# Kernel tuning notes

Hardware: AMD Instinct MI355X
Metric: run time of the kernel (lower is better)

Reference implementation:

```python
import jax, jax.numpy as jnp
import numpy as np
from jax import lax
from jax.scipy.special import logsumexp

TEMP_MIN, TEMP_MAX = 0.1, 1.0
B, I, J, C = 2, 128, 512, 256


def setup_inputs() -> dict:
    key = jax.random.key(0)
    k1, k2, k3 = jax.random.split(key, 3)
    return {
        "text_embeddings": jax.random.normal(k1, (B, I, C), dtype=jnp.float32),
        "mel_embeddings": jax.random.normal(k2, (B, J, C), dtype=jnp.float32),
        "text_mask": jnp.ones((B, I), dtype=jnp.float32),
        "mel_mask": jnp.ones((B, J), dtype=jnp.float32),
        "noise": jax.random.gumbel(k3, (B, I, J), dtype=jnp.float32),  # -log(-log(U))
        "temperature_ratio": jnp.float32(0.5),
    }


def _cond_prob(energy, text_mask, mel_mask, direction):
    # energy: [B, I, J]; returns [B, I, J, K] log conditional probs (normalized over axis 2)
    b, i, j = energy.shape
    if direction == "alpha":
        k = j
        tri = jnp.arange(j)[:, None] >= jnp.arange(k)[None, :]  # triu(ones(J,J)).T layout -> j >= k
        mel_k = mel_mask
    else:  # beta
        k = j - 1
        tri = jnp.arange(j)[:, None] <= jnp.arange(k)[None, :]  # tril(ones(J-1,J)).T layout -> j <= k
        mel_k = mel_mask[:, :k]
    valid = (
        (text_mask[:, :, None, None] * mel_mask[:, None, :, None] * mel_k[:, None, None, :]) > 0
    ) & tri[None, None]
    e4 = jnp.where(valid, energy[..., None], -jnp.inf)  # [B,I,J,K]
    e4 = e4 - logsumexp(e4, axis=2, keepdims=True)
    return jnp.where(valid, e4, jnp.asarray(-10.0, energy.dtype))


def reference(text_embeddings, mel_embeddings, text_mask, mel_mask, noise, temperature_ratio):
    b, i_len, ct = text_embeddings.shape
    j_len, cm = mel_embeddings.shape[1], mel_embeddings.shape[2]
    ninf = jnp.asarray(-jnp.inf, text_embeddings.dtype)

    energy = jnp.einsum("bic,bjc->bij", text_embeddings, mel_embeddings) / np.sqrt(ct * cm)
    temperature = TEMP_MIN + (TEMP_MAX - TEMP_MIN) * temperature_ratio
    energy = (energy + noise) / temperature

    cpa = _cond_prob(energy, text_mask, mel_mask, "alpha")  # [B,I,J,J]
    cpb = _cond_prob(energy, text_mask, mel_mask, "beta")   # [B,I,J,J-1]

    # forward (alpha) recursion over text dim: alpha[:, i, j+1] = LSE_k(alpha[:, i-1, k] + cpa[:, i-1, j, k])
    init_a = jnp.full((b, j_len + 1), -jnp.inf, energy.dtype).at[:, 0].set(0.0)

    def astep(carry, cpa_i):  # carry [B, J+1], cpa_i [B, J, J]
        row = logsumexp(carry[:, None, :-1] + cpa_i, axis=2)  # [B, J]
        new = jnp.concatenate([jnp.full((b, 1), -jnp.inf, energy.dtype), row], axis=1)
        return new, row

    _, arows = lax.scan(astep, init_a, jnp.swapaxes(cpa, 0, 1))
    alpha = jnp.swapaxes(arows, 0, 1)  # [B, I, J] == alpha[:, 1:, 1:]

    # backward (beta) recursion: beta[:, i, j] = LSE_k(beta[:, i+1, k+1] + cpb[:, i, j, k])
    init_b = jnp.full((b, j_len), -jnp.inf, energy.dtype).at[:, -1].set(0.0)

    def bstep(carry, cpb_i):  # carry [B, J], cpb_i [B, J, J-1]
        row = logsumexp(carry[:, None, 1:] + cpb_i, axis=2)
        return row, row

    _, brows = lax.scan(bstep, init_b, jnp.flip(jnp.swapaxes(cpb[:, : i_len - 1], 0, 1), axis=0))
    beta = jnp.concatenate([jnp.flip(brows, axis=0), init_b[None]], axis=0)
    beta = jnp.swapaxes(beta, 0, 1)  # [B, I, J]

    gamma = alpha + beta
    gmask = (text_mask[:, :, None] * mel_mask[:, None, :]) > 0
    gamma = jnp.where(gmask, gamma, ninf)
    gamma = jnp.where(gmask, gamma - logsumexp(gamma, axis=1, keepdims=True), ninf)

    expanded = jnp.einsum("bij,bic->bjc", jnp.exp(gamma), text_embeddings)
    expanded = expanded * mel_mask[:, :, None]
    return gamma, expanded
```

## Files before the change

### kernel.cpp

```cpp
#include <hip/hip_runtime.h>
#include <math.h>

#define BB 2
#define II 128
#define JJ 512
#define CC 256
#define NEL (BB*II*JJ)
#define NINF (-INFINITY)
#define K10 4.5399929762484854e-5f

typedef float f32x4 __attribute__((ext_vector_type(4)));

template<int CTRL, int RM = 0xf, int BM = 0xf, bool BC = true>
__device__ __forceinline__ float dppf(float x) {
    return __int_as_float(__builtin_amdgcn_update_dpp(
        0, __float_as_int(x), CTRL, RM, BM, BC));
}
template<int CTRL, int RM = 0xf, int BM = 0xf>
__device__ __forceinline__ float dppself(float x) {
    return __int_as_float(__builtin_amdgcn_update_dpp(
        __float_as_int(x), __float_as_int(x), CTRL, RM, BM, false));
}
__device__ __forceinline__ float wscan_incl(float x) {
    x += dppf<0x111>(x);
    x += dppf<0x112>(x);
    x += dppf<0x114>(x);
    x += dppf<0x118>(x);
    x += dppf<0x142, 0xa>(x);
    x += dppf<0x143, 0xc>(x);
    return x;
}
__device__ __forceinline__ float wscan_maxf(float x) {
    x = fmaxf(x, dppself<0x111>(x));
    x = fmaxf(x, dppself<0x112>(x));
    x = fmaxf(x, dppself<0x114>(x));
    x = fmaxf(x, dppself<0x118>(x));
    x = fmaxf(x, dppself<0x142, 0xa>(x));
    x = fmaxf(x, dppself<0x143, 0xc>(x));
    return x;
}
__device__ __forceinline__ float lane_shr1(float x) { return dppf<0x138>(x); }
__device__ __forceinline__ float bcast63(float x) {
    return __int_as_float(__builtin_amdgcn_readlane(__float_as_int(x), 63));
}

__device__ __forceinline__ void tree_prefix8(const float x[8], float P[8]) {
    float t[8];
    t[0] = x[0];
    #pragma unroll
    for (int q = 1; q < 8; ++q) t[q] = x[q] + x[q-1];
    float u[8];
    u[0] = t[0]; u[1] = t[1];
    #pragma unroll
    for (int q = 2; q < 8; ++q) u[q] = t[q] + t[q-2];
    P[0] = u[0]; P[1] = u[1]; P[2] = u[2]; P[3] = u[3];
    #pragma unroll
    for (int q = 4; q < 8; ++q) P[q] = u[q] + u[q-4];
}

__device__ __forceinline__ void loadrow8(const float* p, float v[8]) {
    float4 a = *reinterpret_cast<const float4*>(p);
    float4 b = *reinterpret_cast<const float4*>(p + 4);
    v[0]=a.x; v[1]=a.y; v[2]=a.z; v[3]=a.w;
    v[4]=b.x; v[5]=b.y; v[6]=b.z; v[7]=b.w;
}
__device__ __forceinline__ void storerow8(float* __restrict__ p, const float v[8]) {
    *reinterpret_cast<float4*>(p)     = make_float4(v[0],v[1],v[2],v[3]);
    *reinterpret_cast<float4*>(p + 4) = make_float4(v[4],v[5],v[6],v[7]);
}

__device__ __forceinline__ void aload2(f32x4 &d0, f32x4 &d1, const float* p) {
    asm volatile("global_load_dwordx4 %0, %2, off\n\t"
                 "global_load_dwordx4 %1, %2, off offset:16"
                 : "=&v"(d0), "=&v"(d1) : "v"(p) : "memory");
}
__device__ __forceinline__ void astore2(f32x4 d0, f32x4 d1, float* p) {
    asm volatile("global_store_dwordx4 %2, %0, off\n\t"
                 "global_store_dwordx4 %2, %1, off offset:16"
                 :: "v"(d0), "v"(d1), "v"(p) : "memory");
}
template<int N> __device__ __forceinline__ void waitcnt_vm() {
    asm volatile("s_waitcnt vmcnt(%0)" :: "i"(N) : "memory");
}

struct Buf { f32x4 e0, e1; };

__device__ __forceinline__ void preproc(const float ev[8], float CE[8], float CW[8]) {
    float m8 = fmaxf(fmaxf(fmaxf(ev[0],ev[1]), fmaxf(ev[2],ev[3])),
                     fmaxf(fmaxf(ev[4],ev[5]), fmaxf(ev[6],ev[7])));
    float m = bcast63(wscan_maxf(m8));
    float x[8];
    #pragma unroll
    for (int q = 0; q < 8; ++q) x[q] = __expf(ev[q] - m);
    float P[8];
    tree_prefix8(x, P);
    float sc = wscan_incl(P[7]);
    float cp = lane_shr1(sc);
    float T  = bcast63(sc);
    #pragma unroll
    for (int q = 0; q < 8; ++q) {
        CE[q] = x[q];
        CW[q] = __builtin_amdgcn_rcpf(T - (cp + P[q]) + x[q]);
    }
}

__global__ __launch_bounds__(256) void energy_kernel(
        const float* __restrict__ text, const float* __restrict__ mel,
        const float* __restrict__ noise, const float* __restrict__ ratio,
        float* __restrict__ e) {
    __shared__ float melS[64][65];
    __shared__ float texS[8][65];
    int b  = blockIdx.x;
    int i0 = blockIdx.y * 8;
    int j0 = blockIdx.z * 64;
    int t = threadIdx.x;
    int jj = t & 63, ig = t >> 6;
    float acc0 = 0.f, acc1 = 0.f;
    for (int cc = 0; cc < CC; cc += 64) {
        #pragma unroll
        for (int k = 0; k < 4; ++k) {
            int idx = t + k * 256;
            int row = idx >> 4, seg = idx & 15;
            float4 v = *reinterpret_cast<const float4*>(
                mel + (size_t)(b * JJ + j0 + row) * CC + cc + seg * 4);
            melS[row][seg*4+0] = v.x; melS[row][seg*4+1] = v.y;
            melS[row][seg*4+2] = v.z; melS[row][seg*4+3] = v.w;
        }
        if (t < 128) {
            int row = t >> 4, seg = t & 15;
            float4 v = *reinterpret_cast<const float4*>(
                text + (size_t)(b * II + i0 + row) * CC + cc + seg * 4);
            texS[row][seg*4+0] = v.x; texS[row][seg*4+1] = v.y;
            texS[row][seg*4+2] = v.z; texS[row][seg*4+3] = v.w;
        }
        __syncthreads();
        #pragma unroll 8
        for (int c = 0; c < 64; ++c) {
            float m = melS[jj][c];
            acc0 = fmaf(m, texS[ig*2+0][c], acc0);
            acc1 = fmaf(m, texS[ig*2+1][c], acc1);
        }
        __syncthreads();
    }
    float temp = 0.1f + 0.9f * ratio[0];
    float rtmp = 1.0f / temp;
    int r0 = (b * II + i0 + ig*2 + 0) * JJ + j0 + jj;
    int r1 = (b * II + i0 + ig*2 + 1) * JJ + j0 + jj;
    e[r0] = (acc0 * (1.0f/256.0f) + noise[r0]) * rtmp;
    e[r1] = (acc1 * (1.0f/256.0f) + noise[r1]) * rtmp;
}


template<bool NORM, int VM, bool PF>
__device__ __forceinline__ void astep(
    int i, int lane, int off,
    const float (&pin)[8], float (&pout)[8], float& c,
    Buf& B,
    const float* __restrict__ eB,
    float* __restrict__ paB, float* ldsC)
{
    {
        f32x4 s0 = {pin[0], pin[1], pin[2], pin[3]};
        f32x4 s1 = {pin[4], pin[5], pin[6], pin[7]};
        astore2(s0, s1, paB + (size_t)(i - 1) * JJ + off);
    }
    if (lane == 0) ldsC[i - 1] = c;
    waitcnt_vm<VM>();
    __builtin_amdgcn_sched_barrier(0);
    float ev[8] = {B.e0[0],B.e0[1],B.e0[2],B.e0[3],B.e1[0],B.e1[1],B.e1[2],B.e1[3]};
    if (PF) aload2(B.e0, B.e1, eB + (size_t)(i + 5) * JJ + off);
    float CE[8], CW[8];
    preproc(ev, CE, CW);

    float pup = lane_shr1(pin[7]);
    float y[8];
    y[0] = pup * CW[0];
    #pragma unroll
    for (int q = 1; q < 8; ++q) y[q] = pin[q-1] * CW[q];
    float zz[8];
    #pragma unroll
    for (int q = 0; q < 7; ++q) zz[q] = pin[q];
    zz[7] = (lane == 63) ? 0.0f : pin[7];
    float Y[8], Z[8];
    tree_prefix8(y, Y);
    tree_prefix8(zz, Z);
    float sy = wscan_incl(Y[7]);
    float sz = wscan_incl(Z[7]);
    float oy = lane_shr1(sy);
    float oz = lane_shr1(sz);
    float T  = bcast63(sz);
    #pragma unroll
    for (int q = 0; q < 8; ++q) {
        float S1 = oy + Y[q];
        float S2 = fmaxf(T - (oz + Z[q]) + zz[q], 0.0f);
        pout[q] = fmaf(CE[q], S1, K10 * S2);
    }
    if (NORM) {
        float Tc = fmaxf(T, 1e-30f);
        float rT = __builtin_amdgcn_rcpf(Tc);
        c += __logf(Tc);
        #pragma unroll
        for (int q = 0; q < 8; ++q) pout[q] *= rT;
    }
}

template<bool NORM, int VM, bool PF>
__device__ __forceinline__ void bstep(
    int i, int lane, int off,
    const float (&pin)[8], float (&pout)[8], float& c,
    Buf& B,
    const float* __restrict__ eB,
    float* __restrict__ pbB, float* ldsC)
{
    {
        f32x4 s0 = {pin[0], pin[1], pin[2], pin[3]};
        f32x4 s1 = {pin[4], pin[5], pin[6], pin[7]};
        astore2(s0, s1, pbB + (size_t)(i + 1) * JJ + off);
    }
    if (lane == 0) ldsC[i + 1] = c;
    waitcnt_vm<VM>();
    __builtin_amdgcn_sched_barrier(0);
    float ev[8] = {B.e1[3],B.e1[2],B.e1[1],B.e1[0],B.e0[3],B.e0[2],B.e0[1],B.e0[0]};
    if (PF) aload2(B.e0, B.e1, eB + (size_t)(i - 5) * JJ + 504 - 8 * lane);
    float CE[8], CW[8];
    preproc(ev, CE, CW);

    float pup = lane_shr1(pin[7]);
    float pn[8];
    pn[0] = pup;
    #pragma unroll
    for (int q = 1; q < 8; ++q) pn[q] = pin[q-1];
    float w[8];
    #pragma unroll
    for (int q = 0; q < 8; ++q) w[q] = pn[q] * CW[q];
    float W[8], N[8];
    tree_prefix8(w, W);
    tree_prefix8(pn, N);
    float sw = wscan_incl(W[7]);
    float sn = wscan_incl(N[7]);
    float ow = lane_shr1(sw);
    float on = lane_shr1(sn);
    float T  = bcast63(sn);
    #pragma unroll
    for (int q = 0; q < 8; ++q) {
        float QA = ow + W[q];
        float QB = fmaxf(T - (on + N[q]), 0.0f);
        pout[q] = fmaf(CE[q], QA, K10 * QB);
    }
    if (NORM) {
        float Tc = fmaxf(T, 1e-30f);
        float rT = __builtin_amdgcn_rcpf(Tc);
        c += __logf(Tc);
        #pragma unroll
        for (int q = 0; q < 8; ++q) pout[q] *= rT;
    }
}

__global__ __launch_bounds__(64, 1) void scan_ab_kernel(
        const float* __restrict__ e,
        float* __restrict__ pa, float* __restrict__ pb,
        float* __restrict__ ca, float* __restrict__ cb) {
    __shared__ float ldsC[II];
    int b = blockIdx.x >> 1, dir = blockIdx.x & 1;
    int lane = threadIdx.x, off = lane * 8;
    size_t base = (size_t)b * II * JJ;
    float PS0[8],PS1[8],PS2[8],PS3[8],PS4[8],PS5[8],PS6[8],PS7[8],PS8[8],PS9[8];
    Buf B0,B1,B2,B3,B4;
    float c = 0.0f;

    if (dir == 0) {
        const float* eB = e + base;
        float* paB = pa + base; float* caB = ca + b * II;
        float e0r[8];
        loadrow8(eB + off, e0r);
        {
            float m8 = fmaxf(fmaxf(fmaxf(e0r[0],e0r[1]), fmaxf(e0r[2],e0r[3])),
                             fmaxf(fmaxf(e0r[4],e0r[5]), fmaxf(e0r[6],e0r[7])));
            float m = bcast63(wscan_maxf(m8));
            float x0[8];
            #pragma unroll
            for (int q = 0; q < 8; ++q) x0[q] = __expf(e0r[q] - m);
            float P[8];
            tree_prefix8(x0, P);
            float T = bcast63(wscan_incl(P[7]));
            float rT = __builtin_amdgcn_rcpf(T);
            #pragma unroll
            for (int q = 0; q < 8; ++q) PS0[q] = x0[q] * rT;
        }
        __builtin_amdgcn_sched_barrier(0);
        aload2(B1.e0, B1.e1, eB + (size_t)1*JJ + off);
        aload2(B2.e0, B2.e1, eB + (size_t)2*JJ + off);
        aload2(B3.e0, B3.e1, eB + (size_t)3*JJ + off);
        aload2(B4.e0, B4.e1, eB + (size_t)4*JJ + off);
        aload2(B0.e0, B0.e1, eB + (size_t)5*JJ + off);
        astep<true ,10,true>(1, lane, off, PS0, PS1, c, B1, eB, paB, ldsC);
        astep<false,12,true>(2, lane, off, PS1, PS2, c, B2, eB, paB, ldsC);
        astep<false,14,true>(3, lane, off, PS2, PS3, c, B3, eB, paB, ldsC);
        astep<false,16,true>(4, lane, off, PS3, PS4, c, B4, eB, paB, ldsC);
        astep<false,18,true>(5, lane, off, PS4, PS5, c, B0, eB, paB, ldsC);
        #pragma unroll 1
        for (int d = 0; d < 11; ++d) {
            int i = 6 + 10 * d;
            astep<true ,18,true>(i+0, lane, off, PS5, PS6, c, B1, eB, paB, ldsC);
            astep<false,18,true>(i+1, lane, off, PS6, PS7, c, B2, eB, paB, ldsC);
            astep<false,18,true>(i+2, lane, off, PS7, PS8, c, B3, eB, paB, ldsC);
            astep<false,18,true>(i+3, lane, off, PS8, PS9, c, B4, eB, paB, ldsC);
            astep<false,18,true>(i+4, lane, off, PS9, PS0, c, B0, eB, paB, ldsC);
            astep<true ,18,true>(i+5, lane, off, PS0, PS1, c, B1, eB, paB, ldsC);
            astep<false,18,true>(i+6, lane, off, PS1, PS2, c, B2, eB, paB, ldsC);
            astep<false,18,true>(i+7, lane, off, PS2, PS3, c, B3, eB, paB, ldsC);
            astep<false,18,true>(i+8, lane, off, PS3, PS4, c, B4, eB, paB, ldsC);
            astep<false,18,true>(i+9, lane, off, PS4, PS5, c, B0, eB, paB, ldsC);
        }
        astep<true ,18,true>(116, lane, off, PS5, PS6, c, B1, eB, paB, ldsC);
        astep<false,18,true>(117, lane, off, PS6, PS7, c, B2, eB, paB, ldsC);
        astep<false,18,true>(118, lane, off, PS7, PS8, c, B3, eB, paB, ldsC);
        astep<false,18,true>(119, lane, off, PS8, PS9, c, B4, eB, paB, ldsC);
        astep<false,18,true>(120, lane, off, PS9, PS0, c, B0, eB, paB, ldsC);
        astep<true ,18,true>(121, lane, off, PS0, PS1, c, B1, eB, paB, ldsC);
        astep<false,18,true>(122, lane, off, PS1, PS2, c, B2, eB, paB, ldsC);
        astep<false,18,false>(123, lane, off, PS2, PS3, c, B3, eB, paB, ldsC);
        astep<false,16,false>(124, lane, off, PS3, PS4, c, B4, eB, paB, ldsC);
        astep<false,14,false>(125, lane, off, PS4, PS5, c, B0, eB, paB, ldsC);
        astep<true ,12,false>(126, lane, off, PS5, PS6, c, B1, eB, paB, ldsC);
        astep<false,10,false>(127, lane, off, PS6, PS7, c, B2, eB, paB, ldsC);
        storerow8(paB + (size_t)127 * JJ + off, PS7);
        if (lane == 0) ldsC[127] = c;
        waitcnt_vm<0>();
        caB[lane]      = ldsC[lane];
        caB[lane + 64] = ldsC[lane + 64];
    } else {
        const float* eB = e + base;
        float* pbB = pb + base; float* cbB = cb + b * II;
        #pragma unroll
        for (int q = 0; q < 8; ++q) PS7[q] = 0.0f;
        PS7[0] = (lane == 0) ? 1.0f : 0.0f;
        aload2(B1.e0, B1.e1, eB + (size_t)126*JJ + 504 - 8*lane);
        aload2(B0.e0, B0.e1, eB + (size_t)125*JJ + 504 - 8*lane);
        aload2(B4.e0, B4.e1, eB + (size_t)124*JJ + 504 - 8*lane);
        aload2(B3.e0, B3.e1, eB + (size_t)123*JJ + 504 - 8*lane);
        aload2(B2.e0, B2.e1, eB + (size_t)122*JJ + 504 - 8*lane);
        bstep<true ,10,true>(126, lane, off, PS7, PS6, c, B1, eB, pbB, ldsC);
        bstep<false,12,true>(125, lane, off, PS6, PS5, c, B0, eB, pbB, ldsC);
        bstep<false,14,true>(124, lane, off, PS5, PS4, c, B4, eB, pbB, ldsC);
        bstep<false,16,true>(123, lane, off, PS4, PS3, c, B3, eB, pbB, ldsC);
        bstep<false,18,true>(122, lane, off, PS3, PS2, c, B2, eB, pbB, ldsC);
        #pragma unroll 1
        for (int d = 0; d < 11; ++d) {
            int i = 121 - 10 * d;
            bstep<true ,18,true>(i-0, lane, off, PS2, PS1, c, B1, eB, pbB, ldsC);
            bstep<false,18,true>(i-1, lane, off, PS1, PS0, c, B0, eB, pbB, ldsC);
            bstep<false,18,true>(i-2, lane, off, PS0, PS9, c, B4, eB, pbB, ldsC);
            bstep<false,18,true>(i-3, lane, off, PS9, PS8, c, B3, eB, pbB, ldsC);
            bstep<false,18,true>(i-4, lane, off, PS8, PS7, c, B2, eB, pbB, ldsC);
            bstep<true ,18,true>(i-5, lane, off, PS7, PS6, c, B1, eB, pbB, ldsC);
            bstep<false,18,true>(i-6, lane, off, PS6, PS5, c, B0, eB, pbB, ldsC);
            bstep<false,18,true>(i-7, lane, off, PS5, PS4, c, B4, eB, pbB, ldsC);
            bstep<false,18,true>(i-8, lane, off, PS4, PS3, c, B3, eB, pbB, ldsC);
            bstep<false,18,true>(i-9, lane, off, PS3, PS2, c, B2, eB, pbB, ldsC);
        }
        bstep<true ,18,true>(11, lane, off, PS2, PS1, c, B1, eB, pbB, ldsC);
        bstep<false,18,true>(10, lane, off, PS1, PS0, c, B0, eB, pbB, ldsC);
        bstep<false,18,true>( 9, lane, off, PS0, PS9, c, B4, eB, pbB, ldsC);
        bstep<false,18,true>( 8, lane, off, PS9, PS8, c, B3, eB, pbB, ldsC);
        bstep<false,18,true>( 7, lane, off, PS8, PS7, c, B2, eB, pbB, ldsC);
        bstep<true ,18,true>( 6, lane, off, PS7, PS6, c, B1, eB, pbB, ldsC);
        bstep<false,18,true>( 5, lane, off, PS6, PS5, c, B0, eB, pbB, ldsC);
        bstep<false,18,false>(4, lane, off, PS5, PS4, c, B4, eB, pbB, ldsC);
        bstep<false,16,false>(3, lane, off, PS4, PS3, c, B3, eB, pbB, ldsC);
        bstep<false,14,false>(2, lane, off, PS3, PS2, c, B2, eB, pbB, ldsC);
        bstep<true ,12,false>(1, lane, off, PS2, PS1, c, B1, eB, pbB, ldsC);
        bstep<false,10,false>(0, lane, off, PS1, PS0, c, B0, eB, pbB, ldsC);
        storerow8(pbB + off, PS0);
        if (lane == 0) ldsC[0] = c;
        waitcnt_vm<0>();
        cbB[lane]      = ldsC[lane];
        cbB[lane + 64] = ldsC[lane + 64];
    }
}

__global__ __launch_bounds__(256) void gamma_expand_kernel(
        const float* __restrict__ pa, const float* __restrict__ pb,
        const float* __restrict__ ca, const float* __restrict__ cb,
        const float* __restrict__ text, const float* __restrict__ mmask,
        float* __restrict__ gamma_out, float* __restrict__ expanded) {
    __shared__ float wt[II][9];
    __shared__ float Ei[II];
    __shared__ float red[8][33];
    int b   = blockIdx.x >> 6;
    int jj0 = (blockIdx.x & 63) * 8;
    int t = threadIdx.x;
    int q = t & 7, ic = t >> 3;

    if (t < II) Ei[t] = ca[b*II + t] + cb[b*II + t];
    __syncthreads();
    float maxc = Ei[0];
    #pragma unroll 16
    for (int i = 1; i < II; ++i) maxc = fmaxf(maxc, Ei[i]);
    __syncthreads();
    if (t < II) Ei[t] = __expf(Ei[t] - maxc);
    __syncthreads();

    size_t idx0  = (size_t)b * II * JJ + jj0 + q;
    size_t idx0r = (size_t)b * II * JJ + (JJ - 1 - jj0 - q);
    float d = 0.f;
    #pragma unroll
    for (int k = 0; k < 4; ++k) {
        int i = ic * 4 + k;
        float P = pa[idx0 + (size_t)i * JJ] * pb[idx0r + (size_t)i * JJ] * Ei[i];
        wt[i][q] = P;
        d += P;
    }
    red[q][ic] = d;
    __syncthreads();
    if (t < 8) {
        float s = 0.f;
        #pragma unroll
        for (int k = 0; k < 32; ++k) s += red[t][k];
        red[t][32] = 1.0f / fmaxf(s, 1e-37f);
    }
    __syncthreads();
    float rD = red[q][32];
    #pragma unroll
    for (int k = 0; k < 4; ++k) {
        int i = ic * 4 + k;
        float P = wt[i][q] * rD;
        wt[i][q] = P;
        gamma_out[idx0 + (size_t)i * JJ] = fmaxf(__logf(P), -1e30f);
    }
    __syncthreads();

    float acc[8] = {0,0,0,0,0,0,0,0};
    const float* txb = text + (size_t)b * II * CC + t;
    #pragma unroll 4
    for (int i = 0; i < II; ++i) {
        float tv = txb[(size_t)i * CC];
        #pragma unroll
        for (int qq = 0; qq < 8; ++qq) acc[qq] = fmaf(wt[i][qq], tv, acc[qq]);
    }
    #pragma unroll
    for (int qq = 0; qq < 8; ++qq) {
        expanded[(size_t)(b * JJ + jj0 + qq) * CC + t] =
            acc[qq] * mmask[b * JJ + jj0 + qq];
    }
}

extern "C" void kernel_launch(void* const* d_in, const int* in_sizes, int n_in,
                              void* d_out, int out_size, void* d_ws, size_t ws_size,
                              hipStream_t stream) {
    const float* text  = (const float*)d_in[0];
    const float* mel   = (const float*)d_in[1];
    const float* mmask = (const float*)d_in[3];
    const float* noise = (const float*)d_in[4];
    const float* ratio = (const float*)d_in[5];
    float* gamma_out = (float*)d_out;
    float* expanded  = (float*)d_out + NEL;

    float* ws = (float*)d_ws;
    float* e  = ws;
    float* pa = ws +   NEL;
    float* pb = ws + 2*NEL;
    float* ca = ws + 3*NEL;
    float* cb = ws + 3*NEL + BB*II;

    hipLaunchKernelGGL(energy_kernel, dim3(BB, II/8, JJ/64), dim3(256), 0, stream,
                       text, mel, noise, ratio, e);
    hipLaunchKernelGGL(scan_ab_kernel, dim3(BB*2), dim3(64), 0, stream,
                       e, pa, pb, ca, cb);
    hipLaunchKernelGGL(gamma_expand_kernel, dim3(BB*64), dim3(256), 0, stream,
                       pa, pb, ca, cb, text, mmask, gamma_out, expanded);
}
```

Measured before the change: 156.5 us.

## Software-pipeline energy preprocessing one step ahead and deepen row prefetch to seven

The alpha and beta scan steps now compute the exp-based CE/CW coefficients for the next row while the current row's prefix scan runs, using double-buffered coefficient registers. The prefetch ring grows from five to seven row buffers and the unroll period from ten to fourteen steps, so loads are issued eight rows ahead. This takes the exp preprocessing and load latency off the serial dependency chain at the cost of more live VGPRs, which could cause spills in a one-wave-per-block kernel.

After: 156.6 us. Within noise of the previous version (+0.1%).

```diff
diff --git a/kernel.cpp b/kernel.cpp
--- a/kernel.cpp
+++ b/kernel.cpp
@@ -151,11 +151,13 @@
 }
 
 
-template<bool NORM, int VM, bool PF>
+template<bool NORM, int VM, bool PF, bool PP>
 __device__ __forceinline__ void astep(
     int i, int lane, int off,
     const float (&pin)[8], float (&pout)[8], float& c,
     Buf& B,
+    const float (&CEc)[8], const float (&CWc)[8],
+    float (&CEn)[8], float (&CWn)[8],
     const float* __restrict__ eB,
     float* __restrict__ paB, float* ldsC)
 {
@@ -165,18 +167,23 @@
         astore2(s0, s1, paB + (size_t)(i - 1) * JJ + off);
     }
     if (lane == 0) ldsC[i - 1] = c;
-    waitcnt_vm<VM>();
-    __builtin_amdgcn_sched_barrier(0);
-    float ev[8] = {B.e0[0],B.e0[1],B.e0[2],B.e0[3],B.e1[0],B.e1[1],B.e1[2],B.e1[3]};
-    if (PF) aload2(B.e0, B.e1, eB + (size_t)(i + 5) * JJ + off);
-    float CE[8], CW[8];
-    preproc(ev, CE, CW);
+    if constexpr (VM >= 0) {
+        waitcnt_vm<VM>();
+        __builtin_amdgcn_sched_barrier(0);
+    }
+    float ev[8];
+    if (PP) {
+        ev[0]=B.e0[0]; ev[1]=B.e0[1]; ev[2]=B.e0[2]; ev[3]=B.e0[3];
+        ev[4]=B.e1[0]; ev[5]=B.e1[1]; ev[6]=B.e1[2]; ev[7]=B.e1[3];
+    }
+    if (PF) aload2(B.e0, B.e1, eB + (size_t)(i + 8) * JJ + off);
+    if (PP) preproc(ev, CEn, CWn);
 
     float pup = lane_shr1(pin[7]);
     float y[8];
-    y[0] = pup * CW[0];
-    #pragma unroll
-    for (int q = 1; q < 8; ++q) y[q] = pin[q-1] * CW[q];
+    y[0] = pup * CWc[0];
+    #pragma unroll
+    for (int q = 1; q < 8; ++q) y[q] = pin[q-1] * CWc[q];
     float zz[8];
     #pragma unroll
     for (int q = 0; q < 7; ++q) zz[q] = pin[q];
@@ -193,7 +200,7 @@
     for (int q = 0; q < 8; ++q) {
         float S1 = oy + Y[q];
         float S2 = fmaxf(T - (oz + Z[q]) + zz[q], 0.0f);
-        pout[q] = fmaf(CE[q], S1, K10 * S2);
+        pout[q] = fmaf(CEc[q], S1, K10 * S2);
     }
     if (NORM) {
         float Tc = fmaxf(T, 1e-30f);
@@ -204,11 +211,13 @@
     }
 }
 
-template<bool NORM, int VM, bool PF>
+template<bool NORM, int VM, bool PF, bool PP>
 __device__ __forceinline__ void bstep(
     int i, int lane, int off,
     const float (&pin)[8], float (&pout)[8], float& c,
     Buf& B,
+    const float (&CEc)[8], const float (&CWc)[8],
+    float (&CEn)[8], float (&CWn)[8],
     const float* __restrict__ eB,
     float* __restrict__ pbB, float* ldsC)
 {
@@ -218,12 +227,17 @@
         astore2(s0, s1, pbB + (size_t)(i + 1) * JJ + off);
     }
     if (lane == 0) ldsC[i + 1] = c;
-    waitcnt_vm<VM>();
-    __builtin_amdgcn_sched_barrier(0);
-    float ev[8] = {B.e1[3],B.e1[2],B.e1[1],B.e1[0],B.e0[3],B.e0[2],B.e0[1],B.e0[0]};
-    if (PF) aload2(B.e0, B.e1, eB + (size_t)(i - 5) * JJ + 504 - 8 * lane);
-    float CE[8], CW[8];
-    preproc(ev, CE, CW);
+    if constexpr (VM >= 0) {
+        waitcnt_vm<VM>();
+        __builtin_amdgcn_sched_barrier(0);
+    }
+    float ev[8];
+    if (PP) {
+        ev[0]=B.e1[3]; ev[1]=B.e1[2]; ev[2]=B.e1[1]; ev[3]=B.e1[0];
+        ev[4]=B.e0[3]; ev[5]=B.e0[2]; ev[6]=B.e0[1]; ev[7]=B.e0[0];
+    }
+    if (PF) aload2(B.e0, B.e1, eB + (size_t)(i - 8) * JJ + 504 - 8 * lane);
+    if (PP) preproc(ev, CEn, CWn);
 
     float pup = lane_shr1(pin[7]);
     float pn[8];
@@ -232,7 +246,7 @@
     for (int q = 1; q < 8; ++q) pn[q] = pin[q-1];
     float w[8];
     #pragma unroll
-    for (int q = 0; q < 8; ++q) w[q] = pn[q] * CW[q];
+    for (int q = 0; q < 8; ++q) w[q] = pn[q] * CWc[q];
     float W[8], N[8];
     tree_prefix8(w, W);
     tree_prefix8(pn, N);
@@ -245,7 +259,7 @@
     for (int q = 0; q < 8; ++q) {
         float QA = ow + W[q];
         float QB = fmaxf(T - (on + N[q]), 0.0f);
-        pout[q] = fmaf(CE[q], QA, K10 * QB);
+        pout[q] = fmaf(CEc[q], QA, K10 * QB);
     }
     if (NORM) {
         float Tc = fmaxf(T, 1e-30f);
@@ -264,8 +278,10 @@
     int b = blockIdx.x >> 1, dir = blockIdx.x & 1;
     int lane = threadIdx.x, off = lane * 8;
     size_t base = (size_t)b * II * JJ;
-    float PS0[8],PS1[8],PS2[8],PS3[8],PS4[8],PS5[8],PS6[8],PS7[8],PS8[8],PS9[8];
-    Buf B0,B1,B2,B3,B4;
+    float PS0[8],PS1[8],PS2[8],PS3[8],PS4[8],PS5[8],PS6[8],PS7[8],
+          PS8[8],PS9[8],PS10[8],PS11[8],PS12[8],PS13[8];
+    Buf B0,B1,B2,B3,B4,B5,B6;
+    float CEa[8], CWa[8], CEb[8], CWb[8];
     float c = 0.0f;
 
     if (dir == 0) {
@@ -292,39 +308,50 @@
         aload2(B2.e0, B2.e1, eB + (size_t)2*JJ + off);
         aload2(B3.e0, B3.e1, eB + (size_t)3*JJ + off);
         aload2(B4.e0, B4.e1, eB + (size_t)4*JJ + off);
-        aload2(B0.e0, B0.e1, eB + (size_t)5*JJ + off);
-        astep<true ,10,true>(1, lane, off, PS0, PS1, c, B1, eB, paB, ldsC);
-        astep<false,12,true>(2, lane, off, PS1, PS2, c, B2, eB, paB, ldsC);
-        astep<false,14,true>(3, lane, off, PS2, PS3, c, B3, eB, paB, ldsC);
-        astep<false,16,true>(4, lane, off, PS3, PS4, c, B4, eB, paB, ldsC);
-        astep<false,18,true>(5, lane, off, PS4, PS5, c, B0, eB, paB, ldsC);
+        aload2(B5.e0, B5.e1, eB + (size_t)5*JJ + off);
+        aload2(B6.e0, B6.e1, eB + (size_t)6*JJ + off);
+        aload2(B0.e0, B0.e1, eB + (size_t)7*JJ + off);
+        waitcnt_vm<0>();
+        __builtin_amdgcn_sched_barrier(0);
+        {
+            float ev[8] = {B1.e0[0],B1.e0[1],B1.e0[2],B1.e0[3],B1.e1[0],B1.e1[1],B1.e1[2],B1.e1[3]};
+            aload2(B1.e0, B1.e1, eB + (size_t)8*JJ + off);
+            preproc(ev, CEb, CWb);
+        }
+        astep<true , 4,true,true>(1, lane, off, PS0, PS1, c, B2, CEb,CWb, CEa,CWa, eB, paB, ldsC);
+        astep<false, 8,true,true>(2, lane, off, PS1, PS2, c, B3, CEa,CWa, CEb,CWb, eB, paB, ldsC);
+        astep<false,12,true,true>(3, lane, off, PS2, PS3, c, B4, CEb,CWb, CEa,CWa, eB, paB, ldsC);
+        astep<false,16,true,true>(4, lane, off, PS3, PS4, c, B5, CEa,CWa, CEb,CWb, eB, paB, ldsC);
+        astep<false,20,true,true>(5, lane, off, PS4, PS5, c, B6, CEb,CWb, CEa,CWa, eB, paB, ldsC);
+        astep<false,24,true,true>(6, lane, off, PS5, PS6, c, B0, CEa,CWa, CEb,CWb, eB, paB, ldsC);
+        astep<false,26,true,true>(7, lane, off, PS6, PS7, c, B1, CEb,CWb, CEa,CWa, eB, paB, ldsC);
         #pragma unroll 1
-        for (int d = 0; d < 11; ++d) {
-            int i = 6 + 10 * d;
-            astep<true ,18,true>(i+0, lane, off, PS5, PS6, c, B1, eB, paB, ldsC);
-            astep<false,18,true>(i+1, lane, off, PS6, PS7, c, B2, eB, paB, ldsC);
-            astep<false,18,true>(i+2, lane, off, PS7, PS8, c, B3, eB, paB, ldsC);
-            astep<false,18,true>(i+3, lane, off, PS8, PS9, c, B4, eB, paB, ldsC);
-            astep<false,18,true>(i+4, lane, off, PS9, PS0, c, B0, eB, paB, ldsC);
-            astep<true ,18,true>(i+5, lane, off, PS0, PS1, c, B1, eB, paB, ldsC);
-            astep<false,18,true>(i+6, lane, off, PS1, PS2, c, B2, eB, paB, ldsC);
-            astep<false,18,true>(i+7, lane, off, PS2, PS3, c, B3, eB, paB, ldsC);
-            astep<false,18,true>(i+8, lane, off, PS3, PS4, c, B4, eB, paB, ldsC);
-            astep<false,18,true>(i+9, lane, off, PS4, PS5, c, B0, eB, paB, ldsC);
-        }
-        astep<true ,18,true>(116, lane, off, PS5, PS6, c, B1, eB, paB, ldsC);
-        astep<false,18,true>(117, lane, off, PS6, PS7, c, B2, eB, paB, ldsC);
-        astep<false,18,true>(118, lane, off, PS7, PS8, c, B3, eB, paB, ldsC);
-        astep<false,18,true>(119, lane, off, PS8, PS9, c, B4, eB, paB, ldsC);
-        astep<false,18,true>(120, lane, off, PS9, PS0, c, B0, eB, paB, ldsC);
-        astep<true ,18,true>(121, lane, off, PS0, PS1, c, B1, eB, paB, ldsC);
-        astep<false,18,true>(122, lane, off, PS1, PS2, c, B2, eB, paB, ldsC);
-        astep<false,18,false>(123, lane, off, PS2, PS3, c, B3, eB, paB, ldsC);
-        astep<false,16,false>(124, lane, off, PS3, PS4, c, B4, eB, paB, ldsC);
-        astep<false,14,false>(125, lane, off, PS4, PS5, c, B0, eB, paB, ldsC);
-        astep<true ,12,false>(126, lane, off, PS5, PS6, c, B1, eB, paB, ldsC);
-        astep<false,10,false>(127, lane, off, PS6, PS7, c, B2, eB, paB, ldsC);
-        storerow8(paB + (size_t)127 * JJ + off, PS7);
+        for (int d = 0; d < 8; ++d) {
+            int i = 8 + 14 * d;
+            astep<true ,26,true,true>(i+ 0, lane, off, PS7 , PS8 , c, B2, CEa,CWa, CEb,CWb, eB, paB, ldsC);
+            astep<false,26,true,true>(i+ 1, lane, off, PS8 , PS9 , c, B3, CEb,CWb, CEa,CWa, eB, paB, ldsC);
+            astep<false,26,true,true>(i+ 2, lane, off, PS9 , PS10, c, B4, CEa,CWa, CEb,CWb, eB, paB, ldsC);
+            astep<false,26,true,true>(i+ 3, lane, off, PS10, PS11, c, B5, CEb,CWb, CEa,CWa, eB, paB, ldsC);
+            astep<false,26,true,true>(i+ 4, lane, off, PS11, PS12, c, B6, CEa,CWa, CEb,CWb, eB, paB, ldsC);
+            astep<false,26,true,true>(i+ 5, lane, off, PS12, PS13, c, B0, CEb,CWb, CEa,CWa, eB, paB, ldsC);
+            astep<false,26,true,true>(i+ 6, lane, off, PS13, PS0 , c, B1, CEa,CWa, CEb,CWb, eB, paB, ldsC);
+            astep<true ,26,true,true>(i+ 7, lane, off, PS0 , PS1 , c, B2, CEb,CWb, CEa,CWa, eB, paB, ldsC);
+            astep<false,26,true,true>(i+ 8, lane, off, PS1 , PS2 , c, B3, CEa,CWa, CEb,CWb, eB, paB, ldsC);
+            astep<false,26,true,true>(i+ 9, lane, off, PS2 , PS3 , c, B4, CEb,CWb, CEa,CWa, eB, paB, ldsC);
+            astep<false,26,true,true>(i+10, lane, off, PS3 , PS4 , c, B5, CEa,CWa, CEb,CWb, eB, paB, ldsC);
+            astep<false,26,true,true>(i+11, lane, off, PS4 , PS5 , c, B6, CEb,CWb, CEa,CWa, eB, paB, ldsC);
+            astep<false,26,true,true>(i+12, lane, off, PS5 , PS6 , c, B0, CEa,CWa, CEb,CWb, eB, paB, ldsC);
+            astep<false,26,true,true>(i+13, lane, off, PS6 , PS7 , c, B1, CEb,CWb, CEa,CWa, eB, paB, ldsC);
+        }
+        astep<true ,26,false,true >(120, lane, off, PS7 , PS8 , c, B2, CEa,CWa, CEb,CWb, eB, paB, ldsC);
+        astep<false,24,false,true >(121, lane, off, PS8 , PS9 , c, B3, CEb,CWb, CEa,CWa, eB, paB, ldsC);
+        astep<false,22,false,true >(122, lane, off, PS9 , PS10, c, B4, CEa,CWa, CEb,CWb, eB, paB, ldsC);
+        astep<false,20,false,true >(123, lane, off, PS10, PS11, c, B5, CEb,CWb, CEa,CWa, eB, paB, ldsC);
+        astep<false,18,false,true >(124, lane, off, PS11, PS12, c, B6, CEa,CWa, CEb,CWb, eB, paB, ldsC);
+        astep<false,16,false,true >(125, lane, off, PS12, PS13, c, B0, CEb,CWb, CEa,CWa, eB, paB, ldsC);
+        astep<false,14,false,true >(126, lane, off, PS13, PS0 , c, B1, CEa,CWa, CEb,CWb, eB, paB, ldsC);
+        astep<true ,-1,false,false>(127, lane, off, PS0 , PS1 , c, B2, CEb,CWb, CEa,CWa, eB, paB, ldsC);
+        storerow8(paB + (size_t)127 * JJ + off, PS1);
         if (lane == 0) ldsC[127] = c;
         waitcnt_vm<0>();
         caB[lane]      = ldsC[lane];
@@ -333,45 +360,56 @@
         const float* eB = e + base;
         float* pbB = pb + base; float* cbB = cb + b * II;
         #pragma unroll
-        for (int q = 0; q < 8; ++q) PS7[q] = 0.0f;
-        PS7[0] = (lane == 0) ? 1.0f : 0.0f;
-        aload2(B1.e0, B1.e1, eB + (size_t)126*JJ + 504 - 8*lane);
-        aload2(B0.e0, B0.e1, eB + (size_t)125*JJ + 504 - 8*lane);
-        aload2(B4.e0, B4.e1, eB + (size_t)124*JJ + 504 - 8*lane);
-        aload2(B3.e0, B3.e1, eB + (size_t)123*JJ + 504 - 8*lane);
-        aload2(B2.e0, B2.e1, eB + (size_t)122*JJ + 504 - 8*lane);
-        bstep<true ,10,true>(126, lane, off, PS7, PS6, c, B1, eB, pbB, ldsC);
-        bstep<false,12,true>(125, lane, off, PS6, PS5, c, B0, eB, pbB, ldsC);
-        bstep<false,14,true>(124, lane, off, PS5, PS4, c, B4, eB, pbB, ldsC);
-        bstep<false,16,true>(123, lane, off, PS4, PS3, c, B3, eB, pbB, ldsC);
-        bstep<false,18,true>(122, lane, off, PS3, PS2, c, B2, eB, pbB, ldsC);
+        for (int q = 0; q < 8; ++q) PS0[q] = 0.0f;
+        PS0[0] = (lane == 0) ? 1.0f : 0.0f;
+        aload2(B0.e0, B0.e1, eB + (size_t)126*JJ + 504 - 8*lane);
+        aload2(B6.e0, B6.e1, eB + (size_t)125*JJ + 504 - 8*lane);
+        aload2(B5.e0, B5.e1, eB + (size_t)124*JJ + 504 - 8*lane);
+        aload2(B4.e0, B4.e1, eB + (size_t)123*JJ + 504 - 8*lane);
+        aload2(B3.e0, B3.e1, eB + (size_t)122*JJ + 504 - 8*lane);
+        aload2(B2.e0, B2.e1, eB + (size_t)121*JJ + 504 - 8*lane);
+        aload2(B1.e0, B1.e1, eB + (size_t)120*JJ + 504 - 8*lane);
+        waitcnt_vm<0>();
+        __builtin_amdgcn_sched_barrier(0);
+        {
+            float ev[8] = {B0.e1[3],B0.e1[2],B0.e1[1],B0.e1[0],B0.e0[3],B0.e0[2],B0.e0[1],B0.e0[0]};
+            aload2(B0.e0, B0.e1, eB + (size_t)119*JJ + 504 - 8*lane);
+            preproc(ev, CEa, CWa);
+        }
+        bstep<true , 4,true,true>(126, lane, off, PS0, PS1, c, B6, CEa,CWa, CEb,CWb, eB, pbB, ldsC);
+        bstep<false, 8,true,true>(125, lane, off, PS1, PS2, c, B5, CEb,CWb, CEa,CWa, eB, pbB, ldsC);
+        bstep<false,12,true,true>(124, lane, off, PS2, PS3, c, B4, CEa,CWa, CEb,CWb, eB, pbB, ldsC);
+        bstep<false,16,true,true>(123, lane, off, PS3, PS4, c, B3, CEb,CWb, CEa,CWa, eB, pbB, ldsC);
+        bstep<false,20,true,true>(122, lane, off, PS4, PS5, c, B2, CEa,CWa, CEb,CWb, eB, pbB, ldsC);
+        bstep<false,24,true,true>(121, lane, off, PS5, PS6, c, B1, CEb,CWb, CEa,CWa, eB, pbB, ldsC);
+        bstep<false,26,true,true>(120, lane, off, PS6, PS7, c, B0, CEa,CWa, CEb,CWb, eB, pbB, ldsC);
         #pragma unroll 1
-        for (int d = 0; d < 11; ++d) {
-            int i = 121 - 10 * d;
-            bstep<true ,18,true>(i-0, lane, off, PS2, PS1, c, B1, eB, pbB, ldsC);
-            bstep<false,18,true>(i-1, lane, off, PS1, PS0, c, B0, eB, pbB, ldsC);
-            bstep<false,18,true>(i-2, lane, off, PS0, PS9, c, B4, eB, pbB, ldsC);
-            bstep<false,18,true>(i-3, lane, off, PS9, PS8, c, B3, eB, pbB, ldsC);
-            bstep<false,18,true>(i-4, lane, off, PS8, PS7, c, B2, eB, pbB, ldsC);
-            bstep<true ,18,true>(i-5, lane, off, PS7, PS6, c, B1, eB, pbB, ldsC);
-            bstep<false,18,true>(i-6, lane, off, PS6, PS5, c, B0, eB, pbB, ldsC);
-            bstep<false,18,true>(i-7, lane, off, PS5, PS4, c, B4, eB, pbB, ldsC);
-            bstep<false,18,true>(i-8, lane, off, PS4, PS3, c, B3, eB, pbB, ldsC);
-            bstep<false,18,true>(i-9, lane, off, PS3, PS2, c, B2, eB, pbB, ldsC);
-        }
-        bstep<true ,18,true>(11, lane, off, PS2, PS1, c, B1, eB, pbB, ldsC);
-        bstep<false,18,true>(10, lane, off, PS1, PS0, c, B0, eB, pbB, ldsC);
-        bstep<false,18,true>( 9, lane, off, PS0, PS9, c, B4, eB, pbB, ldsC);
-        bstep<false,18,true>( 8, lane, off, PS9, PS8, c, B3, eB, pbB, ldsC);
-        bstep<false,18,true>( 7, lane, off, PS8, PS7, c, B2, eB, pbB, ldsC);
-        bstep<true ,18,true>( 6, lane, off, PS7, PS6, c, B1, eB, pbB, ldsC);
-        bstep<false,18,true>( 5, lane, off, PS6, PS5, c, B0, eB, pbB, ldsC);
-        bstep<false,18,false>(4, lane, off, PS5, PS4, c, B4, eB, pbB, ldsC);
-        bstep<false,16,false>(3, lane, off, PS4, PS3, c, B3, eB, pbB, ldsC);
-        bstep<false,14,false>(2, lane, off, PS3, PS2, c, B2, eB, pbB, ldsC);
-        bstep<true ,12,false>(1, lane, off, PS2, PS1, c, B1, eB, pbB, ldsC);
-        bstep<false,10,false>(0, lane, off, PS1, PS0, c, B0, eB, pbB, ldsC);
-        storerow8(pbB + off, PS0);
+        for (int d = 0; d < 8; ++d) {
+            int i = 119 - 14 * d;
+            bstep<true ,26,true,true>(i- 0, lane, off, PS7 , PS8 , c, B6, CEb,CWb, CEa,CWa, eB, pbB, ldsC);
+            bstep<false,26,true,true>(i- 1, lane, off, PS8 , PS9 , c, B5, CEa,CWa, CEb,CWb, eB, pbB, ldsC);
+            bstep<false,26,true,true>(i- 2, lane, off, PS9 , PS10, c, B4, CEb,CWb, CEa,CWa, eB, pbB, ldsC);
+            bstep<false,26,true,true>(i- 3, lane, off, PS10, PS11, c, B3, CEa,CWa, CEb,CWb, eB, pbB, ldsC);
+            bstep<false,26,true,true>(i- 4, lane, off, PS11, PS12, c, B2, CEb,CWb, CEa,CWa, eB, pbB, ldsC);
+            bstep<false,26,true,true>(i- 5, lane, off, PS12, PS13, c, B1, CEa,CWa, CEb,CWb, eB, pbB, ldsC);
+            bstep<false,26,true,true>(i- 6, lane, off, PS13, PS0 , c, B0, CEb,CWb, CEa,CWa, eB, pbB, ldsC);
+            bstep<true ,26,true,true>(i- 7, lane, off, PS0 , PS1 , c, B6, CEa,CWa, CEb,CWb, eB, pbB, ldsC);
+            bstep<false,26,true,true>(i- 8, lane, off, PS1 , PS2 , c, B5, CEb,CWb, CEa,CWa, eB, pbB, ldsC);
+            bstep<false,26,true,true>(i- 9, lane, off, PS2 , PS3 , c, B4, CEa,CWa, CEb,CWb, eB, pbB, ldsC);
+            bstep<false,26,true,true>(i-10, lane, off, PS3 , PS4 , c, B3, CEb,CWb, CEa,CWa, eB, pbB, ldsC);
+            bstep<false,26,true,true>(i-11, lane, off, PS4 , PS5 , c, B2, CEa,CWa, CEb,CWb, eB, pbB, ldsC);
+            bstep<false,26,true,true>(i-12, lane, off, PS5 , PS6 , c, B1, CEb,CWb, CEa,CWa, eB, pbB, ldsC);
+            bstep<false,26,true,true>(i-13, lane, off, PS6 , PS7 , c, B0, CEa,CWa, CEb,CWb, eB, pbB, ldsC);
+        }
+        bstep<true ,26,false,true >(7, lane, off, PS7 , PS8 , c, B6, CEb,CWb, CEa,CWa, eB, pbB, ldsC);
+        bstep<false,24,false,true >(6, lane, off, PS8 , PS9 , c, B5, CEa,CWa, CEb,CWb, eB, pbB, ldsC);
+        bstep<false,22,false,true >(5, lane, off, PS9 , PS10, c, B4, CEb,CWb, CEa,CWa, eB, pbB, ldsC);
+        bstep<false,20,false,true >(4, lane, off, PS10, PS11, c, B3, CEa,CWa, CEb,CWb, eB, pbB, ldsC);
+        bstep<false,18,false,true >(3, lane, off, PS11, PS12, c, B2, CEb,CWb, CEa,CWa, eB, pbB, ldsC);
+        bstep<false,16,false,true >(2, lane, off, PS12, PS13, c, B1, CEa,CWa, CEb,CWb, eB, pbB, ldsC);
+        bstep<false,14,false,true >(1, lane, off, PS13, PS0 , c, B0, CEb,CWb, CEa,CWa, eB, pbB, ldsC);
+        bstep<true ,-1,false,false>(0, lane, off, PS0 , PS1 , c, B6, CEa,CWa, CEb,CWb, eB, pbB, ldsC);
+        storerow8(pbB + off, PS1);
         if (lane == 0) ldsC[0] = c;
         waitcnt_vm<0>();
         cbB[lane]      = ldsC[lane];
```
